# Optimization experiments

Hardware: AMD Instinct MI355X
Metric: run time of the kernel (lower is better)

## Reference

```python
import jax, jax.numpy as jnp
import numpy as np

D = 512; E = 8; TOPK = 2; F = 2048; H = 4
SF_LEVELS = 4; SF_BASE = 4.0; LN_EPS = 1e-5


def _ln(h, s, b):
    mu = jnp.mean(h, axis=-1, keepdims=True)
    var = jnp.mean((h - mu) ** 2, axis=-1, keepdims=True)
    return (h - mu) / jnp.sqrt(var + LN_EPS) * s + b


def setup_inputs() -> dict:
    key = jax.random.key(0)
    ks = jax.random.split(key, 16)
    sc = 0.02
    inp = {
        "x": jax.random.normal(ks[0], (4, 1024, D), jnp.float32),
        "gate_w": jax.random.normal(ks[1], (D, E), jnp.float32) * sc,
        "gate_b": jnp.zeros((E,), jnp.float32),
        "ln1_s": jnp.ones((E, D), jnp.float32),
        "ln1_b": jnp.zeros((E, D), jnp.float32),
        "ln2_s": jnp.ones((E, D), jnp.float32),
        "ln2_b": jnp.zeros((E, D), jnp.float32),
        "wq": jax.random.normal(ks[2], (E, D, D), jnp.float32) * sc,
        "wk": jax.random.normal(ks[3], (E, D, D), jnp.float32) * sc,
        "wv": jax.random.normal(ks[4], (E, D, D), jnp.float32) * sc,
        "wo": jax.random.normal(ks[5], (E, D, D), jnp.float32) * sc,
        "bq": jnp.zeros((E, D), jnp.float32),
        "bk": jnp.zeros((E, D), jnp.float32),
        "bv": jnp.zeros((E, D), jnp.float32),
        "bo": jnp.zeros((E, D), jnp.float32),
        "w1": jax.random.normal(ks[6], (E, D, F), jnp.float32) * sc,
        "b1": jnp.zeros((E, F), jnp.float32),
        "w2": jax.random.normal(ks[7], (E, F, D), jnp.float32) * sc,
        "b2": jnp.zeros((E, D), jnp.float32),
    }
    return inp


def reference(x, gate_w, gate_b, ln1_s, ln1_b, ln2_s, ln2_b, wq, wk, wv, wo, bq, bk, bv, bo, w1, b1, w2, b2):
    B, S, d = x.shape
    dh = d // H
    # --- SpikingRouter ---
    logits = x @ gate_w + gate_b                       # [B,S,E]
    _, idx = jax.lax.top_k(logits, TOPK)               # [B,S,k]
    in_topk = jnp.sum(jax.nn.one_hot(idx, E, dtype=logits.dtype), axis=-2) > 0
    routing_in = jnp.where(in_topk, jax.nn.relu(logits), 0.0)
    # Scale-and-Fire neuron: multi-level threshold quantization
    mem = routing_in
    rw = jnp.zeros_like(mem)
    for lvl in range(SF_LEVELS):
        thr = SF_BASE / (2.0 ** lvl)
        spk = (mem >= thr).astype(mem.dtype)
        rw = rw + spk * thr
        mem = mem - spk * thr
    # --- all experts (SFormerBlock, post-norm transformer block) ---
    def block(p):
        l1s, l1b, l2s, l2b, Wq, Wk, Wv, Wo, Bq, Bk, Bv, Bo, W1, B1, W2, B2 = p
        q = (x @ Wq + Bq).reshape(B, S, H, dh)
        k = (x @ Wk + Bk).reshape(B, S, H, dh)
        v = (x @ Wv + Bv).reshape(B, S, H, dh)
        scores = jnp.einsum('bqhd,bkhd->bhqk', q, k) / jnp.sqrt(jnp.asarray(dh, x.dtype))
        att = jax.nn.softmax(scores, axis=-1)
        o = jnp.einsum('bhqk,bkhd->bqhd', att, v).reshape(B, S, d) @ Wo + Bo
        h = _ln(x + o, l1s, l1b)
        f = jax.nn.relu(h @ W1 + B1) @ W2 + B2
        return _ln(h + f, l2s, l2b)

    expert_outs = jax.vmap(block)((ln1_s, ln1_b, ln2_s, ln2_b, wq, wk, wv, wo, bq, bk, bv, bo, w1, b1, w2, b2))  # [E,B,S,D]
    final = jnp.einsum('ebsd,bse->bsd', expert_outs, rw)
    return final, logits
```

## Files before the change

### kernel.cpp

```cpp
#include <hip/hip_runtime.h>
#include <hip/hip_bf16.h>
#include <stdint.h>

using u16 = unsigned short;
typedef float floatx4 __attribute__((ext_vector_type(4)));
typedef __bf16 bfv8 __attribute__((ext_vector_type(8)));

#define AS1 __attribute__((address_space(1)))
#define AS3 __attribute__((address_space(3)))

__device__ __forceinline__ u16 f2bf_bits(float f) {
    __hip_bfloat16 h = __float2bfloat16(f);
    u16 u;
    __builtin_memcpy(&u, &h, 2);
    return u;
}
__device__ __forceinline__ float bf_bits2f(u16 u) {
    __hip_bfloat16 h;
    __builtin_memcpy(&h, &u, 2);
    return __bfloat162float(h);
}
__device__ __forceinline__ void gload_lds16(const void* g, void* l) {
    __builtin_amdgcn_global_load_lds((AS1 void*)(uintptr_t)g, (AS3 void*)l, 16, 0, 0);
}

__device__ __forceinline__ void stage64(const u16* __restrict__ Abase, long lda, const long* arow,
                                        const u16* __restrict__ Bb, long ldb, int k0, int tid,
                                        u16* Ad, u16* Bd) {
    #pragma unroll
    for (int j = 0; j < 4; ++j) {
        const int q   = j * 256 + tid;
        const int row = q >> 3;
        const int cg  = (q & 7) ^ (row & 7);
        gload_lds16(Abase + arow[j] * lda + k0 + cg * 8, Ad + q * 8);
        gload_lds16(Bb + (long)row * ldb + k0 + cg * 8, Bd + q * 8);
    }
}
__device__ __forceinline__ void stage_one(const u16* __restrict__ base, long ld, int tid, u16* dst) {
    #pragma unroll
    for (int j = 0; j < 4; ++j) {
        const int q   = j * 256 + tid;
        const int row = q >> 3;
        const int cg  = (q & 7) ^ (row & 7);
        gload_lds16(base + (long)row * ld + cg * 8, dst + q * 8);
    }
}
__device__ __forceinline__ void compute64(const u16* Ab, const u16* Bb, int wy, int wx,
                                          int quad, int mrow, floatx4 acc[4][4]) {
    #pragma unroll
    for (int kk = 0; kk < 2; ++kk) {
        bfv8 af[4], bf[4];
        #pragma unroll
        for (int mi = 0; mi < 4; mi++) {
            const int r = wy * 64 + mi * 16 + mrow;
            const int slot = (kk * 4 + quad) ^ (r & 7);
            af[mi] = *(const bfv8*)&Ab[r * 64 + slot * 8];
        }
        #pragma unroll
        for (int ni = 0; ni < 4; ni++) {
            const int r = wx * 64 + ni * 16 + mrow;
            const int slot = (kk * 4 + quad) ^ (r & 7);
            bf[ni] = *(const bfv8*)&Bb[r * 64 + slot * 8];
        }
        #pragma unroll
        for (int mi = 0; mi < 4; mi++)
            #pragma unroll
            for (int ni = 0; ni < 4; ni++)
                acc[mi][ni] = __builtin_amdgcn_mfma_f32_16x16x32_bf16(af[mi], bf[ni], acc[mi][ni], 0, 0, 0);
    }
}
__device__ __forceinline__ void computeQK(const u16* Kb, const bfv8 qf[2][4], int wy,
                                          int quad, int mrow, floatx4 acc[4][4]) {
    #pragma unroll
    for (int kk = 0; kk < 2; ++kk) {
        bfv8 af[4];
        #pragma unroll
        for (int mi = 0; mi < 4; mi++) {
            const int r = wy * 64 + mi * 16 + mrow;
            const int slot = (kk * 4 + quad) ^ (r & 7);
            af[mi] = *(const bfv8*)&Kb[r * 64 + slot * 8];
        }
        #pragma unroll
        for (int mi = 0; mi < 4; mi++)
            #pragma unroll
            for (int ni = 0; ni < 4; ni++)
                acc[mi][ni] = __builtin_amdgcn_mfma_f32_16x16x32_bf16(af[mi], qf[kk][ni], acc[mi][ni], 0, 0, 0);
    }
}

__global__ void cast_bf16_kernel(const float* __restrict__ in, u16* __restrict__ out, int n4,
                                 const float* __restrict__ bq, const float* __restrict__ bk,
                                 const float* __restrict__ bv, float* __restrict__ pb) {
    if (blockIdx.x >= 2048) {
        int j = (blockIdx.x - 2048) * 256 + threadIdx.x;
        const float* s = j < 4096 ? bq : (j < 8192 ? bk : bv);
        pb[j] = s[j & 4095];
        return;
    }
    int i = blockIdx.x * blockDim.x + threadIdx.x;
    if (i >= n4) return;
    float4 v = ((const float4*)in)[i];
    ushort4 o;
    o.x = f2bf_bits(v.x); o.y = f2bf_bits(v.y); o.z = f2bf_bits(v.z); o.w = f2bf_bits(v.w);
    ((ushort4*)out)[i] = o;
}

__global__ void transpose_cast_kernel(const float* __restrict__ src, u16* __restrict__ dst,
                                      int R, int C, long sSrc, long sDst) {
    __shared__ float tile[32][33];
    const float* s = src + (long)blockIdx.z * sSrc;
    u16* d = dst + (long)blockIdx.z * sDst;
    int c0 = blockIdx.x * 32, r0 = blockIdx.y * 32;
    int tx = threadIdx.x, ty = threadIdx.y;
    #pragma unroll
    for (int i = 0; i < 4; i++)
        tile[ty + 8*i][tx] = s[(long)(r0 + ty + 8*i) * C + c0 + tx];
    __syncthreads();
    #pragma unroll
    for (int i = 0; i < 4; i++)
        d[(long)(c0 + ty + 8*i) * R + r0 + tx] = f2bf_bits(tile[tx][ty + 8*i]);
}

__global__ void transpose_cast4_kernel(const float* __restrict__ w0, const float* __restrict__ w1p,
                                       const float* __restrict__ w2p, const float* __restrict__ w3p,
                                       u16* __restrict__ dst) {
    __shared__ float tile[32][33];
    int z = blockIdx.z;
    const float* s = (z < 8 ? w0 : z < 16 ? w1p : z < 24 ? w2p : w3p) + (long)(z & 7) * 262144;
    u16* d = dst + (long)z * 262144;
    int c0 = blockIdx.x * 32, r0 = blockIdx.y * 32;
    int tx = threadIdx.x, ty = threadIdx.y;
    #pragma unroll
    for (int i = 0; i < 4; i++)
        tile[ty + 8*i][tx] = s[(long)(r0 + ty + 8*i) * 512 + c0 + tx];
    __syncthreads();
    #pragma unroll
    for (int i = 0; i < 4; i++)
        d[(long)(c0 + ty + 8*i) * 512 + r0 + tx] = f2bf_bits(tile[tx][ty + 8*i]);
}

__global__ __launch_bounds__(512)
void router_kernel(const float* __restrict__ x, const float* __restrict__ gw,
                   const float* __restrict__ gb, float* __restrict__ rw,
                   float* __restrict__ logits_out) {
    int row = blockIdx.x;
    int w = threadIdx.x >> 6;
    int lane = threadIdx.x & 63;
    const float* xr = x + (long)row * 512;
    float sum = 0.f;
    #pragma unroll
    for (int i = 0; i < 8; i++) {
        int d = lane + 64 * i;
        sum += xr[d] * gw[d * 8 + w];
    }
    #pragma unroll
    for (int o = 32; o; o >>= 1) sum += __shfl_down(sum, o, 64);
    __shared__ float lg[8];
    if (lane == 0) lg[w] = sum + gb[w];
    __syncthreads();
    if (threadIdx.x == 0) {
        float l[8];
        #pragma unroll
        for (int e = 0; e < 8; e++) l[e] = lg[e];
        int i1 = 0;
        for (int e = 1; e < 8; e++) if (l[e] > l[i1]) i1 = e;
        int i2 = -1;
        for (int e = 0; e < 8; e++) { if (e == i1) continue; if (i2 < 0 || l[e] > l[i2]) i2 = e; }
        for (int e = 0; e < 8; e++) {
            float v = (e == i1 || e == i2) ? (l[e] > 0.f ? l[e] : 0.f) : 0.f;
            float r = 0.f, mem = v;
            #pragma unroll
            for (int lvl = 0; lvl < 4; lvl++) {
                float thr = 4.0f / (float)(1 << lvl);
                if (mem >= thr) { r += thr; mem -= thr; }
            }
            rw[(long)row * 8 + e] = r;
            logits_out[(long)row * 8 + e] = l[e];
        }
    }
}

__global__ __launch_bounds__(256)
void build_lists_kernel(const float* __restrict__ rw, int* __restrict__ prix,
                        int* __restrict__ act, int* __restrict__ smap,
                        int* __restrict__ tmap, int* __restrict__ tt, int* __restrict__ pt) {
    int b = blockIdx.x;
    int t = threadIdx.x, wv = t >> 6, lane = t & 63;
    __shared__ int wsum[4];
    __shared__ int base_sh;
    if (t == 0) base_sh = 0;
    __syncthreads();
    for (int e = 0; e < 8; e++) {
        int r0 = b * 1024 + t * 4;
        int f[4], c = 0;
        #pragma unroll
        for (int i = 0; i < 4; i++) {
            f[i] = (rw[(long)(r0 + i) * 8 + e] != 0.f) ? 1 : 0;
            c += f[i];
        }
        int incl = c;
        #pragma unroll
        for (int o = 1; o < 64; o <<= 1) {
            int n = __shfl_up(incl, o, 64);
            if (lane >= o) incl += n;
        }
        if (lane == 63) wsum[wv] = incl;
        __syncthreads();
        int woff = 0;
        #pragma unroll
        for (int k = 0; k < 4; k++) if (k < wv) woff += wsum[k];
        int tot = wsum[0] + wsum[1] + wsum[2] + wsum[3];
        int excl = incl - c + woff;
        int base = base_sh;
        int slot = excl;
        #pragma unroll
        for (int i = 0; i < 4; i++) {
            int r = r0 + i;
            if (f[i]) {
                int ps = base + slot;
                prix[b * 3072 + ps] = r;
                act[b * 3072 + ps] = 1;
                smap[(long)r * 8 + e] = ps;
                slot++;
            } else {
                smap[(long)r * 8 + e] = -1;
            }
        }
        int pad = (tot + 127) & ~127;
        for (int s = tot + t; s < pad; s += 256) {
            prix[b * 3072 + base + s] = b * 1024;
            act[b * 3072 + base + s] = 0;
        }
        for (int k = t; k < (pad >> 7); k += 256)
            tmap[b * 32 + (base >> 7) + k] = e;
        __syncthreads();
        if (t == 0) base_sh = base + pad;
        __syncthreads();
    }
    if (t == 0) {
        tt[b] = base_sh >> 7;
        pt[b] = base_sh;
    }
}

__global__ __launch_bounds__(256)
void gemm_kv_kernel(const u16* __restrict__ A,
                    const u16* __restrict__ Wkv,
                    u16* __restrict__ CK, u16* __restrict__ CV,
                    const float* __restrict__ biasKV) {
    __shared__ __align__(16) u16 As[2][128 * 64];
    __shared__ __align__(16) u16 Bs[2][128 * 64];
    const int z = blockIdx.z;
    const u16* Bb = Wkv + (long)z * 262144 + (long)blockIdx.x * 128 * 512;

    const int tid = threadIdx.x;
    const int w = tid >> 6, lane = tid & 63;
    const int wy = w >> 1, wx = w & 1;
    const int quad = lane >> 4, mrow = lane & 15;

    long arow[4];
    #pragma unroll
    for (int j = 0; j < 4; ++j) arow[j] = (long)blockIdx.y * 128 + ((j * 256 + tid) >> 3);

    floatx4 acc[4][4];
    #pragma unroll
    for (int i = 0; i < 4; i++)
        #pragma unroll
        for (int j = 0; j < 4; j++)
            acc[i][j] = floatx4{0.f, 0.f, 0.f, 0.f};

    stage64(A, 512, arow, Bb, 512, 0, tid, As[0], Bs[0]);
    for (int it = 0; it < 8; ++it) {
        const int cur = it & 1;
        __syncthreads();
        if (it + 1 < 8)
            stage64(A, 512, arow, Bb, 512, (it + 1) << 6, tid, As[1 - cur], Bs[1 - cur]);
        compute64(As[cur], Bs[cur], wy, wx, quad, mrow, acc);
    }

    const float* biasb = biasKV + (long)z * 512 + blockIdx.x * 128;
    if (z >= 8) {
        u16* Cb = CV + (long)(z - 8) * 2097152;
        #pragma unroll
        for (int ni = 0; ni < 4; ni++) {
            const int colt = wx * 64 + ni * 16 + mrow;
            const int n = blockIdx.x * 128 + colt;
            float bv = biasb[colt];
            #pragma unroll
            for (int mi = 0; mi < 4; mi++) {
                #pragma unroll
                for (int r = 0; r < 4; r++) {
                    const int m = blockIdx.y * 128 + wy * 64 + mi * 16 + quad * 4 + r;
                    float v = acc[mi][ni][r] + bv;
                    long addr = ((long)(((m >> 10) << 2) + (n >> 7)) * 128 + (n & 127)) * 1024 + (m & 1023);
                    Cb[addr] = f2bf_bits(v);
                }
            }
        }
    } else {
        u16* Cb = CK + (long)z * 2097152 + (long)blockIdx.y * 128 * 512 + blockIdx.x * 128;
        #pragma unroll
        for (int ni = 0; ni < 4; ni++) {
            const int col = wx * 64 + ni * 16 + mrow;
            float bv = biasb[col];
            #pragma unroll
            for (int mi = 0; mi < 4; mi++) {
                #pragma unroll
                for (int r = 0; r < 4; r++) {
                    const int row = wy * 64 + mi * 16 + quad * 4 + r;
                    Cb[(long)row * 512 + col] = f2bf_bits(acc[mi][ni][r] + bv);
                }
            }
        }
    }
}

__global__ __launch_bounds__(256, 2)
void attn_fused_kernel(const u16* __restrict__ QP, const u16* __restrict__ Km,
                       const u16* __restrict__ VT, u16* __restrict__ OC,
                       const int* __restrict__ tmap, const int* __restrict__ tt, float alpha) {
    const int tile = blockIdx.x;
    const int bh = blockIdx.y;
    const int b = bh >> 2, h = bh & 3;
    if (tile >= tt[b]) return;
    const int e = tmap[b * 32 + tile];

    __shared__ __align__(16) u16 Bs[2][128 * 64];
    __shared__ __align__(16) u16 Ps[2][128 * 64];
    __shared__ float rs_sh[2][128];

    const int tid = threadIdx.x;
    const int w = tid >> 6, lane = tid & 63;
    const int wy = w >> 1, wx = w & 1;
    const int quad = lane >> 4, mrow = lane & 15;

    const u16* Qbase = QP + ((long)b * 3072 + tile * 128) * 512 + h * 128;
    const u16* Kbase = Km + ((long)e * 4096 + b * 1024) * 512 + h * 128;
    const u16* Vbase = VT + ((long)e * 16 + bh) * 131072;

    stage_one(Qbase, 512, tid, Ps[0]);
    stage_one(Qbase + 64, 512, tid, Ps[1]);
    __syncthreads();
    bfv8 qf[2][2][4];
    #pragma unroll
    for (int c = 0; c < 2; c++)
        #pragma unroll
        for (int kk = 0; kk < 2; kk++)
            #pragma unroll
            for (int ni = 0; ni < 4; ni++) {
                const int r = wx * 64 + ni * 16 + mrow;
                const int slot = (kk * 4 + quad) ^ (r & 7);
                qf[c][kk][ni] = *(const bfv8*)&Ps[c][r * 64 + slot * 8];
            }

    floatx4 acc_o[4][4];
    float rsum[4];
    #pragma unroll
    for (int i = 0; i < 4; i++) {
        rsum[i] = 0.f;
        #pragma unroll
        for (int j = 0; j < 4; j++) acc_o[i][j] = floatx4{0.f, 0.f, 0.f, 0.f};
    }

    for (int kt = 0; kt < 8; ++kt) {
        __syncthreads();
        stage_one(Kbase + (long)kt * 128 * 512,      512, tid, Bs[0]);
        stage_one(Kbase + (long)kt * 128 * 512 + 64, 512, tid, Bs[1]);
        __syncthreads();

        floatx4 acc_s[4][4];
        #pragma unroll
        for (int i = 0; i < 4; i++)
            #pragma unroll
            for (int j = 0; j < 4; j++) acc_s[i][j] = floatx4{0.f, 0.f, 0.f, 0.f};
        computeQK(Bs[0], qf[0], wy, quad, mrow, acc_s);
        computeQK(Bs[1], qf[1], wy, quad, mrow, acc_s);

        #pragma unroll
        for (int mi = 0; mi < 4; mi++)
            #pragma unroll
            for (int ni = 0; ni < 4; ni++)
                #pragma unroll
                for (int r = 0; r < 4; r++) {
                    float p = __expf(acc_s[mi][ni][r] * alpha);
                    acc_s[mi][ni][r] = p;
                    rsum[ni] += p;
                }

        __syncthreads();
        stage_one(Vbase + kt * 128,      1024, tid, Bs[0]);
        stage_one(Vbase + kt * 128 + 64, 1024, tid, Bs[1]);
        u16* Pw = Ps[wy];
        #pragma unroll
        for (int mi = 0; mi < 4; mi++) {
            const int sb = mi * 2 + (quad >> 1);
            #pragma unroll
            for (int ni = 0; ni < 4; ni++) {
                const int q = wx * 64 + ni * 16 + mrow;
                u16* pr = Pw + q * 64 + (sb ^ (q & 7)) * 8 + (quad & 1) * 4;
                #pragma unroll
                for (int r = 0; r < 4; r += 2) {
                    uint32_t pk = (uint32_t)f2bf_bits(acc_s[mi][ni][r]) |
                                  ((uint32_t)f2bf_bits(acc_s[mi][ni][r + 1]) << 16);
                    *(uint32_t*)(pr + r) = pk;
                }
            }
        }
        __syncthreads();
        compute64(Bs[0], Ps[0], wy, wx, quad, mrow, acc_o);
        compute64(Bs[1], Ps[1], wy, wx, quad, mrow, acc_o);
    }

    #pragma unroll
    for (int ni = 0; ni < 4; ni++) {
        float v = rsum[ni];
        v += __shfl_xor(v, 16, 64);
        v += __shfl_xor(v, 32, 64);
        if (quad == 0) rs_sh[wy][wx * 64 + ni * 16 + mrow] = v;
    }
    __syncthreads();
    u16* Cb = OC + ((long)b * 3072 + tile * 128) * 512 + h * 128;
    #pragma unroll
    for (int ni = 0; ni < 4; ni++) {
        const int q = wx * 64 + ni * 16 + mrow;
        const float inv = 1.f / (rs_sh[0][q] + rs_sh[1][q]);
        #pragma unroll
        for (int mi = 0; mi < 4; mi++) {
            ushort4 st;
            st.x = f2bf_bits(acc_o[mi][ni][0] * inv);
            st.y = f2bf_bits(acc_o[mi][ni][1] * inv);
            st.z = f2bf_bits(acc_o[mi][ni][2] * inv);
            st.w = f2bf_bits(acc_o[mi][ni][3] * inv);
            *(ushort4*)(Cb + (long)q * 512 + wy * 64 + mi * 16 + quad * 4) = st;
        }
    }
}

template<bool RELU, bool GATHER>
__global__ __launch_bounds__(256)
void gemm_packed_kernel(const u16* __restrict__ A, int lda,
                        const u16* __restrict__ B, int ldb, long sBe,
                        u16* __restrict__ C, int ldc,
                        const float* __restrict__ bias, long sBiasE,
                        const int* __restrict__ tmap, const int* __restrict__ tt, int K,
                        const int* __restrict__ prix) {
    const int b = blockIdx.y / 24, tile = blockIdx.y % 24;
    if (tile >= tt[b]) return;
    const int e = tmap[b * 32 + tile];
    __shared__ __align__(16) u16 As[2][128 * 64];
    __shared__ __align__(16) u16 Bs[2][128 * 64];
    const long rbase = (long)b * 3072 + tile * 128;
    const u16* Ab = GATHER ? A : A + rbase * lda;
    const u16* Bb = B + (long)e * sBe + (long)blockIdx.x * 128 * ldb;

    const int tid = threadIdx.x;
    const int w = tid >> 6, lane = tid & 63;
    const int wy = w >> 1, wx = w & 1;
    const int quad = lane >> 4, mrow = lane & 15;

    long arow[4];
    #pragma unroll
    for (int j = 0; j < 4; ++j) {
        const int lr = (j * 256 + tid) >> 3;
        arow[j] = GATHER ? (long)prix[b * 3072 + tile * 128 + lr] : (long)lr;
    }

    floatx4 acc[4][4];
    #pragma unroll
    for (int i = 0; i < 4; i++)
        #pragma unroll
        for (int j = 0; j < 4; j++)
            acc[i][j] = floatx4{0.f, 0.f, 0.f, 0.f};

    const int nk = K >> 6;
    stage64(Ab, lda, arow, Bb, ldb, 0, tid, As[0], Bs[0]);
    for (int it = 0; it < nk; ++it) {
        const int cur = it & 1;
        __syncthreads();
        if (it + 1 < nk)
            stage64(Ab, lda, arow, Bb, ldb, (it + 1) << 6, tid, As[1 - cur], Bs[1 - cur]);
        compute64(As[cur], Bs[cur], wy, wx, quad, mrow, acc);
    }

    u16* Cb = C + rbase * ldc + (long)blockIdx.x * 128;
    const float* biasb = bias + (long)e * sBiasE + blockIdx.x * 128;
    #pragma unroll
    for (int ni = 0; ni < 4; ni++) {
        const int col = wx * 64 + ni * 16 + mrow;
        float bv = biasb[col];
        #pragma unroll
        for (int mi = 0; mi < 4; mi++) {
            #pragma unroll
            for (int r = 0; r < 4; r++) {
                const int row = wy * 64 + mi * 16 + quad * 4 + r;
                float v = acc[mi][ni][r] + bv;
                if (RELU) v = fmaxf(v, 0.f);
                Cb[(long)row * ldc + col] = f2bf_bits(v);
            }
        }
    }
}

__global__ __launch_bounds__(128)
void ln1_kernel(const float* __restrict__ x, const u16* __restrict__ tc,
                const int* __restrict__ prix, const int* __restrict__ act,
                const int* __restrict__ tmap, const int* __restrict__ pt,
                const float* __restrict__ s_all, const float* __restrict__ b_all,
                u16* __restrict__ hb) {
    int blk = blockIdx.x;
    int b = blk / 3072, pslot = blk % 3072;
    if (pslot >= pt[b]) return;
    long row = (long)b * 3072 + pslot;
    int tid = threadIdx.x, w = tid >> 6, lane = tid & 63;
    if (!act[row]) {
        *(ushort4*)(hb + row * 512 + tid * 4) = make_ushort4(0, 0, 0, 0);
        return;
    }
    int r = prix[row];
    int e = tmap[b * 32 + (pslot >> 7)];
    float4 xv = *(const float4*)(x + (long)r * 512 + tid * 4);
    ushort4 tu = *(const ushort4*)(tc + row * 512 + tid * 4);
    float v[4] = {xv.x + bf_bits2f(tu.x), xv.y + bf_bits2f(tu.y),
                  xv.z + bf_bits2f(tu.z), xv.w + bf_bits2f(tu.w)};
    float sum = v[0] + v[1] + v[2] + v[3];
    #pragma unroll
    for (int o = 32; o; o >>= 1) sum += __shfl_down(sum, o, 64);
    __shared__ float sh[4];
    if (lane == 0) sh[w] = sum;
    __syncthreads();
    float mu = (sh[0] + sh[1]) * (1.f / 512.f);
    float sq = 0.f;
    #pragma unroll
    for (int j = 0; j < 4; j++) { float d = v[j] - mu; sq += d * d; }
    #pragma unroll
    for (int o = 32; o; o >>= 1) sq += __shfl_down(sq, o, 64);
    if (lane == 0) sh[2 + w] = sq;
    __syncthreads();
    float inv = 1.f / sqrtf((sh[2] + sh[3]) * (1.f / 512.f) + 1e-5f);
    float4 sv = *(const float4*)(s_all + e * 512 + tid * 4);
    float4 bv = *(const float4*)(b_all + e * 512 + tid * 4);
    ushort4 ub;
    ub.x = f2bf_bits((v[0] - mu) * inv * sv.x + bv.x);
    ub.y = f2bf_bits((v[1] - mu) * inv * sv.y + bv.y);
    ub.z = f2bf_bits((v[2] - mu) * inv * sv.z + bv.z);
    ub.w = f2bf_bits((v[3] - mu) * inv * sv.w + bv.w);
    *(ushort4*)(hb + row * 512 + tid * 4) = ub;
}

__global__ __launch_bounds__(128)
void ln2acc_kernel(const u16* __restrict__ hb, const u16* __restrict__ t2,
                   const float* __restrict__ s_all, const float* __restrict__ b_all,
                   const float* __restrict__ rw, const int* __restrict__ smap,
                   float* __restrict__ out) {
    long r = blockIdx.x;
    int b = (int)(r >> 10);
    int tid = threadIdx.x, w = tid >> 6, lane = tid & 63;
    __shared__ float sh[4];
    float4 acc = make_float4(0.f, 0.f, 0.f, 0.f);
    for (int e = 0; e < 8; e++) {
        int ps = smap[r * 8 + e];
        if (ps >= 0) {
            float wgt = rw[r * 8 + e];
            long row = (long)b * 3072 + ps;
            ushort4 hu = *(const ushort4*)(hb + row * 512 + tid * 4);
            ushort4 fu = *(const ushort4*)(t2 + row * 512 + tid * 4);
            float v[4] = {bf_bits2f(hu.x) + bf_bits2f(fu.x), bf_bits2f(hu.y) + bf_bits2f(fu.y),
                          bf_bits2f(hu.z) + bf_bits2f(fu.z), bf_bits2f(hu.w) + bf_bits2f(fu.w)};
            float sum = v[0] + v[1] + v[2] + v[3];
            #pragma unroll
            for (int o = 32; o; o >>= 1) sum += __shfl_down(sum, o, 64);
            if (lane == 0) sh[w] = sum;
            __syncthreads();
            float mu = (sh[0] + sh[1]) * (1.f / 512.f);
            float sq = 0.f;
            #pragma unroll
            for (int j = 0; j < 4; j++) { float d = v[j] - mu; sq += d * d; }
            #pragma unroll
            for (int o = 32; o; o >>= 1) sq += __shfl_down(sq, o, 64);
            if (lane == 0) sh[2 + w] = sq;
            __syncthreads();
            float inv = 1.f / sqrtf((sh[2] + sh[3]) * (1.f / 512.f) + 1e-5f);
            float4 sv = *(const float4*)(s_all + e * 512 + tid * 4);
            float4 bv = *(const float4*)(b_all + e * 512 + tid * 4);
            acc.x += wgt * ((v[0] - mu) * inv * sv.x + bv.x);
            acc.y += wgt * ((v[1] - mu) * inv * sv.y + bv.y);
            acc.z += wgt * ((v[2] - mu) * inv * sv.z + bv.z);
            acc.w += wgt * ((v[3] - mu) * inv * sv.w + bv.w);
            __syncthreads();
        }
    }
    *(float4*)(out + r * 512 + tid * 4) = acc;
}

static const size_t WB_B   = 0;
static const size_t RW_B   = 50331648;
static const size_t PB_B   = 50462720;
static const size_t TT_B   = 50511872;
static const size_t PT_B   = 50511888;
static const size_t TMAP_B = 50511904;
static const size_t PRIX_B = 50512416;
static const size_t ACT_B  = 50561568;
static const size_t SMAP_B = 50610720;
static const size_t XB_B   = 50741792;
static const size_t Q8_B   = 54936096;
static const size_t K8_B   = 88490528;
static const size_t VT_B   = 122044960;
static const size_t S_B    = 155599392;
static const size_t OC_B   = Q8_B;
static const size_t TC_B   = K8_B;
static const size_t HB_B   = Q8_B;
static const size_t MID_B  = S_B;
static const size_t T2_B   = VT_B;

extern "C" void kernel_launch(void* const* d_in, const int* in_sizes, int n_in,
                              void* d_out, int out_size, void* d_ws, size_t ws_size,
                              hipStream_t stream) {
    const float* x      = (const float*)d_in[0];
    const float* gate_w = (const float*)d_in[1];
    const float* gate_b = (const float*)d_in[2];
    const float* ln1_s  = (const float*)d_in[3];
    const float* ln1_b  = (const float*)d_in[4];
    const float* ln2_s  = (const float*)d_in[5];
    const float* ln2_b  = (const float*)d_in[6];
    const float* wq = (const float*)d_in[7];
    const float* wk = (const float*)d_in[8];
    const float* wv = (const float*)d_in[9];
    const float* wo = (const float*)d_in[10];
    const float* bo = (const float*)d_in[14];
    const float* w1 = (const float*)d_in[15];
    const float* b1 = (const float*)d_in[16];
    const float* w2 = (const float*)d_in[17];
    const float* b2 = (const float*)d_in[18];
    float* out = (float*)d_out;

    char* ws = (char*)d_ws;
    u16*   WB   = (u16*)(ws + WB_B);
    float* RW   = (float*)(ws + RW_B);
    float* PB   = (float*)(ws + PB_B);
    int*   TT   = (int*)(ws + TT_B);
    int*   PT   = (int*)(ws + PT_B);
    int*   TMAP = (int*)(ws + TMAP_B);
    int*   PRIX = (int*)(ws + PRIX_B);
    int*   ACT  = (int*)(ws + ACT_B);
    int*   SMAP = (int*)(ws + SMAP_B);
    u16*   XB   = (u16*)(ws + XB_B);
    u16*   QP   = (u16*)(ws + Q8_B);
    u16*   K8   = (u16*)(ws + K8_B);
    u16*   VT8  = (u16*)(ws + VT_B);
    u16*   OC   = (u16*)(ws + OC_B);
    u16*   TC   = (u16*)(ws + TC_B);
    u16*   HB   = (u16*)(ws + HB_B);
    u16*   MID  = (u16*)(ws + MID_B);
    u16*   T2   = (u16*)(ws + T2_B);

    cast_bf16_kernel<<<dim3(2096), 256, 0, stream>>>(x, XB, 4096 * 512 / 4,
                                                     (const float*)d_in[11], (const float*)d_in[12],
                                                     (const float*)d_in[13], PB);
    transpose_cast4_kernel<<<dim3(16,16,32), dim3(32,8), 0, stream>>>(wq, wk, wv, wo, WB);
    transpose_cast_kernel<<<dim3(64,16,8), dim3(32,8), 0, stream>>>(w1, WB + 8388608,  512,  2048, 1048576, 1048576);
    transpose_cast_kernel<<<dim3(16,64,8), dim3(32,8), 0, stream>>>(w2, WB + 16777216, 2048, 512,  1048576, 1048576);
    router_kernel<<<4096, 512, 0, stream>>>(x, gate_w, gate_b, RW, out + 2097152);
    build_lists_kernel<<<4, 256, 0, stream>>>(RW, PRIX, ACT, SMAP, TMAP, TT, PT);

    const float isq = 0.08838834764831845f;

    gemm_kv_kernel<<<dim3(4,32,16), 256, 0, stream>>>(XB, WB + 2097152, K8, VT8, PB + 4096);
    gemm_packed_kernel<false, true><<<dim3(4,96), 256, 0, stream>>>(
        XB, 512, WB, 512, 262144, QP, 512, PB, 512, TMAP, TT, 512, PRIX);

    attn_fused_kernel<<<dim3(24, 16), 256, 0, stream>>>(QP, K8, VT8, OC, TMAP, TT, isq);

    gemm_packed_kernel<false, false><<<dim3(4,96), 256, 0, stream>>>(
        OC, 512, WB + 6291456, 512, 262144, TC, 512, bo, 512, TMAP, TT, 512, nullptr);
    ln1_kernel<<<12288, 128, 0, stream>>>(x, TC, PRIX, ACT, TMAP, PT, ln1_s, ln1_b, HB);
    gemm_packed_kernel<true, false><<<dim3(16,96), 256, 0, stream>>>(
        HB, 512, WB + 8388608, 512, 1048576, MID, 2048, b1, 2048, TMAP, TT, 512, nullptr);
    gemm_packed_kernel<false, false><<<dim3(4,96), 256, 0, stream>>>(
        MID, 2048, WB + 16777216, 2048, 1048576, T2, 512, b2, 512, TMAP, TT, 2048, nullptr);
    ln2acc_kernel<<<4096, 128, 0, stream>>>(HB, T2, ln2_s, ln2_b, RW, SMAP, out);
}
```

Measured before the change: 434.8 us.

## Merge weight transposes, fuse KV and Q projections, split-K the FFN2 GEMM

Merges the three weight transpose launches into one flat-grid kernel. The KV projection and the gathered Q projection now run in one launch so their blocks fill the GPU together. The FFN2 GEMM is split along K into two halves that write fp32 partials, and ln2acc sums the partials and adds the bias, which doubles the block count for a K=2048 GEMM that had few tiles. The cost is extra fp32 partial traffic, a larger workspace, and one more input to the final layernorm kernel.

Result: slower. 448.8 us (+3.2%).

```diff
diff --git a/kernel.cpp b/kernel.cpp
--- a/kernel.cpp
+++ b/kernel.cpp
@@ -105,12 +105,31 @@
     ((ushort4*)out)[i] = o;
 }
 
-__global__ void transpose_cast_kernel(const float* __restrict__ src, u16* __restrict__ dst,
-                                      int R, int C, long sSrc, long sDst) {
+__global__ void transpose_all_kernel(const float* __restrict__ wq, const float* __restrict__ wk,
+                                     const float* __restrict__ wv, const float* __restrict__ wo,
+                                     const float* __restrict__ w1, const float* __restrict__ w2,
+                                     u16* __restrict__ WB) {
     __shared__ float tile[32][33];
-    const float* s = src + (long)blockIdx.z * sSrc;
-    u16* d = dst + (long)blockIdx.z * sDst;
-    int c0 = blockIdx.x * 32, r0 = blockIdx.y * 32;
+    const int bid = blockIdx.x;
+    const float* s; u16* d; int R, C, c0, r0;
+    if (bid < 8192) {
+        int x = bid & 15, y = (bid >> 4) & 15, z = bid >> 8;
+        s = (z < 8 ? wq : z < 16 ? wk : z < 24 ? wv : wo) + (long)(z & 7) * 262144;
+        d = WB + (long)z * 262144;
+        R = 512; C = 512; c0 = x * 32; r0 = y * 32;
+    } else if (bid < 16384) {
+        int idx = bid - 8192;
+        int x = idx & 63, y = (idx >> 6) & 15, z = idx >> 10;
+        s = w1 + (long)z * 1048576;
+        d = WB + 8388608 + (long)z * 1048576;
+        R = 512; C = 2048; c0 = x * 32; r0 = y * 32;
+    } else {
+        int idx = bid - 16384;
+        int x = idx & 15, y = (idx >> 4) & 63, z = idx >> 10;
+        s = w2 + (long)z * 1048576;
+        d = WB + 16777216 + (long)z * 1048576;
+        R = 2048; C = 512; c0 = x * 32; r0 = y * 32;
+    }
     int tx = threadIdx.x, ty = threadIdx.y;
     #pragma unroll
     for (int i = 0; i < 4; i++)
@@ -119,24 +138,6 @@
     #pragma unroll
     for (int i = 0; i < 4; i++)
         d[(long)(c0 + ty + 8*i) * R + r0 + tx] = f2bf_bits(tile[tx][ty + 8*i]);
-}
-
-__global__ void transpose_cast4_kernel(const float* __restrict__ w0, const float* __restrict__ w1p,
-                                       const float* __restrict__ w2p, const float* __restrict__ w3p,
-                                       u16* __restrict__ dst) {
-    __shared__ float tile[32][33];
-    int z = blockIdx.z;
-    const float* s = (z < 8 ? w0 : z < 16 ? w1p : z < 24 ? w2p : w3p) + (long)(z & 7) * 262144;
-    u16* d = dst + (long)z * 262144;
-    int c0 = blockIdx.x * 32, r0 = blockIdx.y * 32;
-    int tx = threadIdx.x, ty = threadIdx.y;
-    #pragma unroll
-    for (int i = 0; i < 4; i++)
-        tile[ty + 8*i][tx] = s[(long)(r0 + ty + 8*i) * 512 + c0 + tx];
-    __syncthreads();
-    #pragma unroll
-    for (int i = 0; i < 4; i++)
-        d[(long)(c0 + ty + 8*i) * 512 + r0 + tx] = f2bf_bits(tile[tx][ty + 8*i]);
 }
 
 __global__ __launch_bounds__(512)
@@ -244,61 +245,112 @@
 }
 
 __global__ __launch_bounds__(256)
-void gemm_kv_kernel(const u16* __restrict__ A,
-                    const u16* __restrict__ Wkv,
-                    u16* __restrict__ CK, u16* __restrict__ CV,
-                    const float* __restrict__ biasKV) {
+void gemm_kvq_kernel(const u16* __restrict__ XB, const u16* __restrict__ Wkv,
+                     u16* __restrict__ CK, u16* __restrict__ CV,
+                     const float* __restrict__ biasKV,
+                     const u16* __restrict__ Wq, u16* __restrict__ QP,
+                     const float* __restrict__ biasQ,
+                     const int* __restrict__ tmap, const int* __restrict__ tt,
+                     const int* __restrict__ prix) {
     __shared__ __align__(16) u16 As[2][128 * 64];
     __shared__ __align__(16) u16 Bs[2][128 * 64];
-    const int z = blockIdx.z;
-    const u16* Bb = Wkv + (long)z * 262144 + (long)blockIdx.x * 128 * 512;
-
     const int tid = threadIdx.x;
     const int w = tid >> 6, lane = tid & 63;
     const int wy = w >> 1, wx = w & 1;
     const int quad = lane >> 4, mrow = lane & 15;
-
-    long arow[4];
-    #pragma unroll
-    for (int j = 0; j < 4; ++j) arow[j] = (long)blockIdx.y * 128 + ((j * 256 + tid) >> 3);
-
-    floatx4 acc[4][4];
-    #pragma unroll
-    for (int i = 0; i < 4; i++)
-        #pragma unroll
-        for (int j = 0; j < 4; j++)
-            acc[i][j] = floatx4{0.f, 0.f, 0.f, 0.f};
-
-    stage64(A, 512, arow, Bb, 512, 0, tid, As[0], Bs[0]);
-    for (int it = 0; it < 8; ++it) {
-        const int cur = it & 1;
-        __syncthreads();
-        if (it + 1 < 8)
-            stage64(A, 512, arow, Bb, 512, (it + 1) << 6, tid, As[1 - cur], Bs[1 - cur]);
-        compute64(As[cur], Bs[cur], wy, wx, quad, mrow, acc);
-    }
-
-    const float* biasb = biasKV + (long)z * 512 + blockIdx.x * 128;
-    if (z >= 8) {
-        u16* Cb = CV + (long)(z - 8) * 2097152;
-        #pragma unroll
-        for (int ni = 0; ni < 4; ni++) {
-            const int colt = wx * 64 + ni * 16 + mrow;
-            const int n = blockIdx.x * 128 + colt;
-            float bv = biasb[colt];
-            #pragma unroll
-            for (int mi = 0; mi < 4; mi++) {
+    const int bid = blockIdx.x;
+
+    if (bid < 2048) {
+        const int bx = bid & 3, by = (bid >> 2) & 31, z = bid >> 7;
+        const u16* Bb = Wkv + (long)z * 262144 + (long)bx * 128 * 512;
+
+        long arow[4];
+        #pragma unroll
+        for (int j = 0; j < 4; ++j) arow[j] = (long)by * 128 + ((j * 256 + tid) >> 3);
+
+        floatx4 acc[4][4];
+        #pragma unroll
+        for (int i = 0; i < 4; i++)
+            #pragma unroll
+            for (int j = 0; j < 4; j++)
+                acc[i][j] = floatx4{0.f, 0.f, 0.f, 0.f};
+
+        stage64(XB, 512, arow, Bb, 512, 0, tid, As[0], Bs[0]);
+        for (int it = 0; it < 8; ++it) {
+            const int cur = it & 1;
+            __syncthreads();
+            if (it + 1 < 8)
+                stage64(XB, 512, arow, Bb, 512, (it + 1) << 6, tid, As[1 - cur], Bs[1 - cur]);
+            compute64(As[cur], Bs[cur], wy, wx, quad, mrow, acc);
+        }
+
+        const float* biasb = biasKV + (long)z * 512 + bx * 128;
+        if (z >= 8) {
+            u16* Cb = CV + (long)(z - 8) * 2097152;
+            #pragma unroll
+            for (int ni = 0; ni < 4; ni++) {
+                const int colt = wx * 64 + ni * 16 + mrow;
+                const int n = bx * 128 + colt;
+                float bv = biasb[colt];
                 #pragma unroll
-                for (int r = 0; r < 4; r++) {
-                    const int m = blockIdx.y * 128 + wy * 64 + mi * 16 + quad * 4 + r;
-                    float v = acc[mi][ni][r] + bv;
-                    long addr = ((long)(((m >> 10) << 2) + (n >> 7)) * 128 + (n & 127)) * 1024 + (m & 1023);
-                    Cb[addr] = f2bf_bits(v);
+                for (int mi = 0; mi < 4; mi++) {
+                    #pragma unroll
+                    for (int r = 0; r < 4; r++) {
+                        const int m = by * 128 + wy * 64 + mi * 16 + quad * 4 + r;
+                        float v = acc[mi][ni][r] + bv;
+                        long addr = ((long)(((m >> 10) << 2) + (n >> 7)) * 128 + (n & 127)) * 1024 + (m & 1023);
+                        Cb[addr] = f2bf_bits(v);
+                    }
                 }
             }
+        } else {
+            u16* Cb = CK + (long)z * 2097152 + (long)by * 128 * 512 + bx * 128;
+            #pragma unroll
+            for (int ni = 0; ni < 4; ni++) {
+                const int col = wx * 64 + ni * 16 + mrow;
+                float bv = biasb[col];
+                #pragma unroll
+                for (int mi = 0; mi < 4; mi++) {
+                    #pragma unroll
+                    for (int r = 0; r < 4; r++) {
+                        const int row = wy * 64 + mi * 16 + quad * 4 + r;
+                        Cb[(long)row * 512 + col] = f2bf_bits(acc[mi][ni][r] + bv);
+                    }
+                }
+            }
         }
     } else {
-        u16* Cb = CK + (long)z * 2097152 + (long)blockIdx.y * 128 * 512 + blockIdx.x * 128;
+        const int idx = bid - 2048;
+        const int bx = idx & 3, yy = idx >> 2;
+        const int b = yy / 24, tile = yy % 24;
+        if (tile >= tt[b]) return;
+        const int e = tmap[b * 32 + tile];
+        const long rbase = (long)b * 3072 + tile * 128;
+        const u16* Bb = Wq + (long)e * 262144 + (long)bx * 128 * 512;
+
+        long arow[4];
+        #pragma unroll
+        for (int j = 0; j < 4; ++j)
+            arow[j] = (long)prix[b * 3072 + tile * 128 + ((j * 256 + tid) >> 3)];
+
+        floatx4 acc[4][4];
+        #pragma unroll
+        for (int i = 0; i < 4; i++)
+            #pragma unroll
+            for (int j = 0; j < 4; j++)
+                acc[i][j] = floatx4{0.f, 0.f, 0.f, 0.f};
+
+        stage64(XB, 512, arow, Bb, 512, 0, tid, As[0], Bs[0]);
+        for (int it = 0; it < 8; ++it) {
+            const int cur = it & 1;
+            __syncthreads();
+            if (it + 1 < 8)
+                stage64(XB, 512, arow, Bb, 512, (it + 1) << 6, tid, As[1 - cur], Bs[1 - cur]);
+            compute64(As[cur], Bs[cur], wy, wx, quad, mrow, acc);
+        }
+
+        u16* Cb = QP + rbase * 512 + bx * 128;
+        const float* biasb = biasQ + bx * 128;
         #pragma unroll
         for (int ni = 0; ni < 4; ni++) {
             const int col = wx * 64 + ni * 16 + mrow;
@@ -436,21 +488,20 @@
     }
 }
 
-template<bool RELU, bool GATHER>
+template<bool RELU>
 __global__ __launch_bounds__(256)
 void gemm_packed_kernel(const u16* __restrict__ A, int lda,
                         const u16* __restrict__ B, int ldb, long sBe,
                         u16* __restrict__ C, int ldc,
                         const float* __restrict__ bias, long sBiasE,
-                        const int* __restrict__ tmap, const int* __restrict__ tt, int K,
-                        const int* __restrict__ prix) {
+                        const int* __restrict__ tmap, const int* __restrict__ tt, int K) {
     const int b = blockIdx.y / 24, tile = blockIdx.y % 24;
     if (tile >= tt[b]) return;
     const int e = tmap[b * 32 + tile];
     __shared__ __align__(16) u16 As[2][128 * 64];
     __shared__ __align__(16) u16 Bs[2][128 * 64];
     const long rbase = (long)b * 3072 + tile * 128;
-    const u16* Ab = GATHER ? A : A + rbase * lda;
+    const u16* Ab = A + rbase * lda;
     const u16* Bb = B + (long)e * sBe + (long)blockIdx.x * 128 * ldb;
 
     const int tid = threadIdx.x;
@@ -460,10 +511,7 @@
 
     long arow[4];
     #pragma unroll
-    for (int j = 0; j < 4; ++j) {
-        const int lr = (j * 256 + tid) >> 3;
-        arow[j] = GATHER ? (long)prix[b * 3072 + tile * 128 + lr] : (long)lr;
-    }
+    for (int j = 0; j < 4; ++j) arow[j] = (j * 256 + tid) >> 3;
 
     floatx4 acc[4][4];
     #pragma unroll
@@ -496,6 +544,60 @@
                 float v = acc[mi][ni][r] + bv;
                 if (RELU) v = fmaxf(v, 0.f);
                 Cb[(long)row * ldc + col] = f2bf_bits(v);
+            }
+        }
+    }
+}
+
+__global__ __launch_bounds__(256)
+void gemm_ffn2_half_kernel(const u16* __restrict__ MID, const u16* __restrict__ W2T,
+                           float* __restrict__ P0, float* __restrict__ P1,
+                           const int* __restrict__ tmap, const int* __restrict__ tt) {
+    const int b = blockIdx.y / 24, tile = blockIdx.y % 24;
+    if (tile >= tt[b]) return;
+    const int e = tmap[b * 32 + tile];
+    __shared__ __align__(16) u16 As[2][128 * 64];
+    __shared__ __align__(16) u16 Bs[2][128 * 64];
+    const long rbase = (long)b * 3072 + tile * 128;
+    const int koff = blockIdx.z * 1024;
+    const u16* Ab = MID + rbase * 2048 + koff;
+    const u16* Bb = W2T + (long)e * 1048576 + (long)blockIdx.x * 128 * 2048 + koff;
+
+    const int tid = threadIdx.x;
+    const int w = tid >> 6, lane = tid & 63;
+    const int wy = w >> 1, wx = w & 1;
+    const int quad = lane >> 4, mrow = lane & 15;
+
+    long arow[4];
+    #pragma unroll
+    for (int j = 0; j < 4; ++j) arow[j] = (j * 256 + tid) >> 3;
+
+    floatx4 acc[4][4];
+    #pragma unroll
+    for (int i = 0; i < 4; i++)
+        #pragma unroll
+        for (int j = 0; j < 4; j++)
+            acc[i][j] = floatx4{0.f, 0.f, 0.f, 0.f};
+
+    stage64(Ab, 2048, arow, Bb, 2048, 0, tid, As[0], Bs[0]);
+    for (int it = 0; it < 16; ++it) {
+        const int cur = it & 1;
+        __syncthreads();
+        if (it + 1 < 16)
+            stage64(Ab, 2048, arow, Bb, 2048, (it + 1) << 6, tid, As[1 - cur], Bs[1 - cur]);
+        compute64(As[cur], Bs[cur], wy, wx, quad, mrow, acc);
+    }
+
+    float* Cb = (blockIdx.z ? P1 : P0) + rbase * 512 + (long)blockIdx.x * 128;
+    #pragma unroll
+    for (int ni = 0; ni < 4; ni++) {
+        const int col = wx * 64 + ni * 16 + mrow;
+        #pragma unroll
+        for (int mi = 0; mi < 4; mi++) {
+            #pragma unroll
+            for (int r = 0; r < 4; r++) {
+                const int row = wy * 64 + mi * 16 + quad * 4 + r;
+                Cb[(long)row * 512 + col] = acc[mi][ni][r];
             }
         }
     }
@@ -548,7 +650,8 @@
 }
 
 __global__ __launch_bounds__(128)
-void ln2acc_kernel(const u16* __restrict__ hb, const u16* __restrict__ t2,
+void ln2acc_kernel(const u16* __restrict__ hb, const float* __restrict__ p0,
+                   const float* __restrict__ p1, const float* __restrict__ b2,
                    const float* __restrict__ s_all, const float* __restrict__ b_all,
                    const float* __restrict__ rw, const int* __restrict__ smap,
                    float* __restrict__ out) {
@@ -563,9 +666,13 @@
             float wgt = rw[r * 8 + e];
             long row = (long)b * 3072 + ps;
             ushort4 hu = *(const ushort4*)(hb + row * 512 + tid * 4);
-            ushort4 fu = *(const ushort4*)(t2 + row * 512 + tid * 4);
-            float v[4] = {bf_bits2f(hu.x) + bf_bits2f(fu.x), bf_bits2f(hu.y) + bf_bits2f(fu.y),
-                          bf_bits2f(hu.z) + bf_bits2f(fu.z), bf_bits2f(hu.w) + bf_bits2f(fu.w)};
+            float4 f0 = *(const float4*)(p0 + row * 512 + tid * 4);
+            float4 f1 = *(const float4*)(p1 + row * 512 + tid * 4);
+            float4 bb = *(const float4*)(b2 + (long)e * 512 + tid * 4);
+            float v[4] = {bf_bits2f(hu.x) + f0.x + f1.x + bb.x,
+                          bf_bits2f(hu.y) + f0.y + f1.y + bb.y,
+                          bf_bits2f(hu.z) + f0.z + f1.z + bb.z,
+                          bf_bits2f(hu.w) + f0.w + f1.w + bb.w};
             float sum = v[0] + v[1] + v[2] + v[3];
             #pragma unroll
             for (int o = 32; o; o >>= 1) sum += __shfl_down(sum, o, 64);
@@ -610,7 +717,8 @@
 static const size_t TC_B   = K8_B;
 static const size_t HB_B   = Q8_B;
 static const size_t MID_B  = S_B;
-static const size_t T2_B   = VT_B;
+static const size_t FP0_B  = VT_B;
+static const size_t FP1_B  = 205931040;
 
 extern "C" void kernel_launch(void* const* d_in, const int* in_sizes, int n_in,
                               void* d_out, int out_size, void* d_ws, size_t ws_size,
@@ -651,31 +759,29 @@
     u16*   TC   = (u16*)(ws + TC_B);
     u16*   HB   = (u16*)(ws + HB_B);
     u16*   MID  = (u16*)(ws + MID_B);
-    u16*   T2   = (u16*)(ws + T2_B);
+    float* FP0  = (float*)(ws + FP0_B);
+    float* FP1  = (float*)(ws + FP1_B);
 
     cast_bf16_kernel<<<dim3(2096), 256, 0, stream>>>(x, XB, 4096 * 512 / 4,
                                                      (const float*)d_in[11], (const float*)d_in[12],
                                                      (const float*)d_in[13], PB);
-    transpose_cast4_kernel<<<dim3(16,16,32), dim3(32,8), 0, stream>>>(wq, wk, wv, wo, WB);
-    transpose_cast_kernel<<<dim3(64,16,8), dim3(32,8), 0, stream>>>(w1, WB + 8388608,  512,  2048, 1048576, 1048576);
-    transpose_cast_kernel<<<dim3(16,64,8), dim3(32,8), 0, stream>>>(w2, WB + 16777216, 2048, 512,  1048576, 1048576);
+    transpose_all_kernel<<<dim3(24576), dim3(32,8), 0, stream>>>(wq, wk, wv, wo, w1, w2, WB);
     router_kernel<<<4096, 512, 0, stream>>>(x, gate_w, gate_b, RW, out + 2097152);
     build_lists_kernel<<<4, 256, 0, stream>>>(RW, PRIX, ACT, SMAP, TMAP, TT, PT);
 
     const float isq = 0.08838834764831845f;
 
-    gemm_kv_kernel<<<dim3(4,32,16), 256, 0, stream>>>(XB, WB + 2097152, K8, VT8, PB + 4096);
-    gemm_packed_kernel<false, true><<<dim3(4,96), 256, 0, stream>>>(
-        XB, 512, WB, 512, 262144, QP, 512, PB, 512, TMAP, TT, 512, PRIX);
+    gemm_kvq_kernel<<<dim3(2432), 256, 0, stream>>>(
+        XB, WB + 2097152, K8, VT8, PB + 4096, WB, QP, PB, TMAP, TT, PRIX);
 
     attn_fused_kernel<<<dim3(24, 16), 256, 0, stream>>>(QP, K8, VT8, OC, TMAP, TT, isq);
 
-    gemm_packed_kernel<false, false><<<dim3(4,96), 256, 0, stream>>>(
-        OC, 512, WB + 6291456, 512, 262144, TC, 512, bo, 512, TMAP, TT, 512, nullptr);
+    gemm_packed_kernel<false><<<dim3(4,96), 256, 0, stream>>>(
+        OC, 512, WB + 6291456, 512, 262144, TC, 512, bo, 512, TMAP, TT, 512);
     ln1_kernel<<<12288, 128, 0, stream>>>(x, TC, PRIX, ACT, TMAP, PT, ln1_s, ln1_b, HB);
-    gemm_packed_kernel<true, false><<<dim3(16,96), 256, 0, stream>>>(
-        HB, 512, WB + 8388608, 512, 1048576, MID, 2048, b1, 2048, TMAP, TT, 512, nullptr);
-    gemm_packed_kernel<false, false><<<dim3(4,96), 256, 0, stream>>>(
-        MID, 2048, WB + 16777216, 2048, 1048576, T2, 512, b2, 512, TMAP, TT, 2048, nullptr);
-    ln2acc_kernel<<<4096, 128, 0, stream>>>(HB, T2, ln2_s, ln2_b, RW, SMAP, out);
-}
+    gemm_packed_kernel<true><<<dim3(16,96), 256, 0, stream>>>(
+        HB, 512, WB + 8388608, 512, 1048576, MID, 2048, b1, 2048, TMAP, TT, 512);
+    gemm_ffn2_half_kernel<<<dim3(4,96,2), 256, 0, stream>>>(
+        MID, WB + 16777216, FP0, FP1, TMAP, TT);
+    ln2acc_kernel<<<4096, 128, 0, stream>>>(HB, FP0, FP1, b2, ln2_s, ln2_b, RW, SMAP, out);
+}
```
